# Kernel tuning notes

Measured on AMD Instinct MI355X. Metric: run time of the kernel, lower is better.

Reference implementation:

```python
import jax, jax.numpy as jnp
import numpy as np

N_BLOCK = 3; EMBED = 256; N_HEAD = 8; HEAD = EMBED // N_HEAD
N_AGENT = 8; SEQ = 256; BATCH = 64; ACT_DIM = 32
DECAY_SCALE = 1.0
EPS = 1e-6


def _decay_matrix():
    # Per-head decay kappas as in Mava Sable, decay over timesteps (pos // n_agent), causal mask.
    gammas = (1.0 - jnp.exp(jnp.linspace(jnp.log(1.0 / 32.0), jnp.log(1.0 / 512.0), N_HEAD))) * DECAY_SCALE
    t = (jnp.arange(SEQ) // N_AGENT).astype(jnp.float32)
    diff = t[:, None] - t[None, :]
    causal = jnp.arange(SEQ)[:, None] >= jnp.arange(SEQ)[None, :]
    return jnp.where(causal[None], gammas[:, None, None] ** diff[None], 0.0)  # [H,S,S]


def rmsnorm(x, scale):
    return x * jax.lax.rsqrt(jnp.mean(x * x, -1, keepdims=True) + EPS) * scale


def groupnorm(x, scale, bias):
    # GroupNorm with n_head groups over the feature dim, per position.
    B, S, E = x.shape
    xg = x.reshape(B, S, N_HEAD, HEAD)
    mu = xg.mean(-1, keepdims=True)
    var = ((xg - mu) ** 2).mean(-1, keepdims=True)
    xn = ((xg - mu) * jax.lax.rsqrt(var + 1e-5)).reshape(B, S, E)
    return xn * scale + bias


def retention(q_in, k_in, v_in, wq, wk, wv, wg, wo, gns, gnb, decay):
    # Parallel multi-scale retention: (Q K^T * D) V, groupnorm, swish gate from query input.
    B, S, E = q_in.shape
    q = (q_in @ wq).reshape(B, S, N_HEAD, HEAD).transpose(0, 2, 1, 3)
    k = (k_in @ wk).reshape(B, S, N_HEAD, HEAD).transpose(0, 2, 1, 3) / jnp.sqrt(jnp.float32(HEAD))
    v = (v_in @ wv).reshape(B, S, N_HEAD, HEAD).transpose(0, 2, 1, 3)
    scores = jnp.einsum('bhnd,bhmd->bhnm', q, k) * decay[None]
    ret = jnp.einsum('bhnm,bhmd->bhnd', scores, v)
    ret = groupnorm(ret.transpose(0, 2, 1, 3).reshape(B, S, E), gns, gnb)
    return (jax.nn.swish(q_in @ wg) * ret) @ wo


def swiglu(x, wg, w1, w2):
    return (jax.nn.swish(x @ wg) * (x @ w1)) @ w2


def forward(action, obs_rep, w_enc, ln0, wq1, wk1, wv1, wg1, wo1, gns1, gnb1, ln1,
            wq2, wk2, wv2, wg2, wo2, gns2, gnb2, ln2, swg, sw1, sw2, ln3,
            hw1, hb1, hln, hw2, hb2):
    decay = _decay_matrix()
    x = rmsnorm(jax.nn.gelu(action @ w_enc), ln0)
    for b in range(N_BLOCK):
        r1 = retention(x, x, x, wq1[b], wk1[b], wv1[b], wg1[b], wo1[b], gns1[b], gnb1[b], decay)
        x = rmsnorm(x + r1, ln1[b])
        r2 = retention(obs_rep, x, x, wq2[b], wk2[b], wv2[b], wg2[b], wo2[b], gns2[b], gnb2[b], decay)
        x = rmsnorm(obs_rep + r2, ln2[b])
        x = rmsnorm(x + swiglu(x, swg[b], sw1[b], sw2[b]), ln3[b])
    h = rmsnorm(jax.nn.gelu(x @ hw1 + hb1), hln)
    return h @ hw2 + hb2


def setup_inputs() -> dict:
    key = jax.random.key(0)
    ks = jax.random.split(key, 24)
    E, A, NB = EMBED, ACT_DIM, N_BLOCK
    s = 0.02
    return {
        'action': jax.random.uniform(ks[0], (BATCH, SEQ, A), jnp.float32),
        'obs_rep': jax.random.normal(ks[1], (BATCH, SEQ, E), jnp.float32),
        'w_enc': jax.random.normal(ks[2], (A, E), jnp.float32) * s,
        'ln0': jnp.ones((E,), jnp.float32),
        'wq1': jax.random.normal(ks[3], (NB, E, E), jnp.float32) * s,
        'wk1': jax.random.normal(ks[4], (NB, E, E), jnp.float32) * s,
        'wv1': jax.random.normal(ks[5], (NB, E, E), jnp.float32) * s,
        'wg1': jax.random.normal(ks[6], (NB, E, E), jnp.float32) * s,
        'wo1': jax.random.normal(ks[7], (NB, E, E), jnp.float32) * s,
        'gns1': jnp.ones((NB, E), jnp.float32),
        'gnb1': jnp.zeros((NB, E), jnp.float32),
        'ln1': jnp.ones((NB, E), jnp.float32),
        'wq2': jax.random.normal(ks[8], (NB, E, E), jnp.float32) * s,
        'wk2': jax.random.normal(ks[9], (NB, E, E), jnp.float32) * s,
        'wv2': jax.random.normal(ks[10], (NB, E, E), jnp.float32) * s,
        'wg2': jax.random.normal(ks[11], (NB, E, E), jnp.float32) * s,
        'wo2': jax.random.normal(ks[12], (NB, E, E), jnp.float32) * s,
        'gns2': jnp.ones((NB, E), jnp.float32),
        'gnb2': jnp.zeros((NB, E), jnp.float32),
        'ln2': jnp.ones((NB, E), jnp.float32),
        'swg': jax.random.normal(ks[13], (NB, E, E), jnp.float32) * s,
        'sw1': jax.random.normal(ks[14], (NB, E, E), jnp.float32) * s,
        'sw2': jax.random.normal(ks[15], (NB, E, E), jnp.float32) * s,
        'ln3': jnp.ones((NB, E), jnp.float32),
        'hw1': jax.random.normal(ks[16], (E, E), jnp.float32) * s,
        'hb1': jnp.zeros((E,), jnp.float32),
        'hln': jnp.ones((E,), jnp.float32),
        'hw2': jax.random.normal(ks[17], (E, A), jnp.float32) * s,
        'hb2': jnp.zeros((A,), jnp.float32),
    }


def reference(action, obs_rep, w_enc, ln0, wq1, wk1, wv1, wg1, wo1, gns1, gnb1, ln1,
              wq2, wk2, wv2, wg2, wo2, gns2, gnb2, ln2, swg, sw1, sw2, ln3,
              hw1, hb1, hln, hw2, hb2):
    return forward(action, obs_rep, w_enc, ln0, wq1, wk1, wv1, wg1, wo1, gns1, gnb1, ln1,
                   wq2, wk2, wv2, wg2, wo2, gns2, gnb2, ln2, swg, sw1, sw2, ln3,
                   hw1, hb1, hln, hw2, hb2)
```

## Files before the change

kernel.cpp:

```cpp
#include <hip/hip_runtime.h>
#include <cstdint>
#include <cmath>

typedef __attribute__((ext_vector_type(8))) short short8;
typedef __attribute__((ext_vector_type(4))) float floatx4;

#define DEV static __device__ __forceinline__

DEV float bf2f(uint16_t u) {
    union { uint32_t i; float f; } v; v.i = ((uint32_t)u) << 16; return v.f;
}
DEV uint16_t f2bf(float f) {
    union { float f; uint32_t i; } v; v.f = f;
    uint32_t r = (v.i + 0x7FFFu + ((v.i >> 16) & 1u)) >> 16;
    return (uint16_t)r;
}
DEV float swishf(float x) { return x / (1.f + __expf(-x)); }
DEV float geluf(float x) {
    const float c = 0.7978845608028654f;
    float t = tanhf(c * (x + 0.044715f * x * x * x));
    return 0.5f * x * (1.f + t);
}

#define CHUNK_E 8192
#define MAT_E   65536
#define APAD    264


struct TArg { const float* src[15]; };

__global__ __launch_bounds__(256) void tpose_k(TArg ta, uint16_t* __restrict__ arena) {
    int z = blockIdx.z;
    const float* src; uint16_t* dst;
    if (z == 0) {
        if (blockIdx.y) return;
        src = ta.src[0]; dst = arena;
    } else if (z <= 39) {
        int q = z - 1; int ti = q / 3, s = q % 3;
        src = ta.src[1 + ti] + (size_t)s * 65536;
        dst = arena + CHUNK_E + (size_t)(ti * 3 + s) * MAT_E;
    } else {
        src = ta.src[14]; dst = arena + CHUNK_E + (size_t)39 * MAT_E;
    }
    int k0 = blockIdx.y << 5;
    int n0 = blockIdx.x << 6;
    __shared__ __align__(16) uint16_t tile[32][72];
    int t = threadIdx.x;
    {
        int r = t >> 3, c = (t & 7) << 3;
        const float* s0 = src + (size_t)(k0 + r) * 256 + n0 + c;
        float4 f0 = *(const float4*)s0;
        float4 f1 = *(const float4*)(s0 + 4);
        tile[r][c + 0] = f2bf(f0.x); tile[r][c + 1] = f2bf(f0.y);
        tile[r][c + 2] = f2bf(f0.z); tile[r][c + 3] = f2bf(f0.w);
        tile[r][c + 4] = f2bf(f1.x); tile[r][c + 5] = f2bf(f1.y);
        tile[r][c + 6] = f2bf(f1.z); tile[r][c + 7] = f2bf(f1.w);
    }
    __syncthreads();
    {
        int n = t >> 2, c = (t & 3) << 3;
        uint16_t tmp[8];
#pragma unroll
        for (int j = 0; j < 8; ++j) tmp[j] = tile[c + j][n];
        *(uint4*)&dst[(size_t)(k0 >> 5) * CHUNK_E + (size_t)(n0 + n) * 32 + c] = *(uint4*)tmp;
    }
}

struct SegArgs {
    const float* action; const float* obs;
    uint16_t *actb, *obsb, *xb, *bq, *bk, *bv, *bg, *brg;
    const float *ln0, *hb1, *hln, *hw2, *hb2;
    float* outp;
    float l2g[8];
};

enum { EP_NONE = 0, EP_GELU_RMS = 1, EP_RESID_RMS = 2 };
enum { EP2_NONE = 0, EP2_SWIGLU = 1 };

template<int EPI, int K, int LDA, bool OG, int LDO, bool RL>
DEV void gemm_u(int m0,
                const uint16_t* __restrict__ A,
                const uint16_t* __restrict__ Wt,
                uint16_t* __restrict__ Og,
                uint16_t* __restrict__ Ol,
                const float* __restrict__ bias,
                const uint16_t* __restrict__ Rg,
                const uint16_t* __restrict__ Rl,
                const float* __restrict__ lnw,
                float (&rowsum)[8][32])
{
    const int t = threadIdx.x;
    const int w = t >> 6, lane = t & 63, l16 = lane & 15, lg = lane >> 4;
    constexpr int NC = K / 32;

    floatx4 acc[2][2];
#pragma unroll
    for (int i = 0; i < 2; ++i)
#pragma unroll
        for (int j = 0; j < 2; ++j) acc[i][j] = (floatx4){0.f, 0.f, 0.f, 0.f};

#pragma unroll
    for (int kc = 0; kc < NC; ++kc) {
        short8 aF[2], bF[2];
#pragma unroll
        for (int rt = 0; rt < 2; ++rt) {
            int row = (rt << 4) + l16;
            if constexpr (LDA != 0)
                aF[rt] = *(const short8*)(A + (size_t)row * LDA + (kc << 5) + (lg << 3));
            else
                aF[rt] = *(const short8*)(A + (size_t)(m0 + row) * K + (kc << 5) + (lg << 3));
        }
#pragma unroll
        for (int ct = 0; ct < 2; ++ct)
            bF[ct] = *(const short8*)(Wt + (size_t)kc * CHUNK_E +
                                      (size_t)((w << 5) + (ct << 4) + l16) * 32 + (lg << 3));
#pragma unroll
        for (int rt = 0; rt < 2; ++rt)
#pragma unroll
            for (int ct = 0; ct < 2; ++ct)
                acc[rt][ct] = __builtin_amdgcn_mfma_f32_16x16x32_bf16(
                    aF[rt], bF[ct], acc[rt][ct], 0, 0, 0);
    }

    float v[2][2][4];
#pragma unroll
    for (int rt = 0; rt < 2; ++rt)
#pragma unroll
        for (int ct = 0; ct < 2; ++ct)
#pragma unroll
            for (int r = 0; r < 4; ++r) {
                int row = (rt << 4) + (lg << 2) + r;
                int col = (w << 5) + (ct << 4) + l16;
                float x = acc[rt][ct][r];
                if constexpr (EPI == EP_GELU_RMS) {
                    if (bias) x += bias[col];
                    x = geluf(x);
                }
                if constexpr (EPI == EP_RESID_RMS) {
                    if constexpr (RL) x += bf2f(Rl[(size_t)row * APAD + col]);
                    else              x += bf2f(Rg[(size_t)(m0 + row) * 256 + col]);
                }
                v[rt][ct][r] = x;
            }

    if constexpr (EPI == EP_GELU_RMS || EPI == EP_RESID_RMS) {
#pragma unroll
        for (int rt = 0; rt < 2; ++rt)
#pragma unroll
            for (int r = 0; r < 4; ++r) {
                float p = v[rt][0][r] * v[rt][0][r] + v[rt][1][r] * v[rt][1][r];
                p += __shfl_xor(p, 1, 64); p += __shfl_xor(p, 2, 64);
                p += __shfl_xor(p, 4, 64); p += __shfl_xor(p, 8, 64);
                int row = (rt << 4) + (lg << 2) + r;
                if (l16 == 0) rowsum[w][row] = p;
            }
        __syncthreads();
#pragma unroll
        for (int rt = 0; rt < 2; ++rt)
#pragma unroll
            for (int r = 0; r < 4; ++r) {
                int row = (rt << 4) + (lg << 2) + r;
                float tot = rowsum[0][row] + rowsum[1][row] + rowsum[2][row] + rowsum[3][row]
                          + rowsum[4][row] + rowsum[5][row] + rowsum[6][row] + rowsum[7][row];
                float rn = rsqrtf(tot * (1.f / 256.f) + 1e-6f);
#pragma unroll
                for (int ct = 0; ct < 2; ++ct) {
                    int col = (w << 5) + (ct << 4) + l16;
                    uint16_t bb = f2bf(v[rt][ct][r] * rn * lnw[col]);
                    if constexpr (OG)
                        Og[(size_t)(m0 + row) * 256 + col] = bb;
                    if constexpr (LDO != 0)
                        Ol[(size_t)row * LDO + col] = bb;
                }
            }
        __syncthreads();
    } else {
#pragma unroll
        for (int rt = 0; rt < 2; ++rt)
#pragma unroll
            for (int ct = 0; ct < 2; ++ct)
#pragma unroll
                for (int r = 0; r < 4; ++r) {
                    int row = (rt << 4) + (lg << 2) + r;
                    int col = (w << 5) + (ct << 4) + l16;
                    uint16_t bb = f2bf(v[rt][ct][r]);
                    if constexpr (OG)
                        Og[(size_t)(m0 + row) * 256 + col] = bb;
                    if constexpr (LDO != 0)
                        Ol[(size_t)row * LDO + col] = bb;
                }
    }
}

template<int EPI, int LDA>
DEV void gemm2_u(int m0, const uint16_t* __restrict__ A,
                 const uint16_t* __restrict__ W1, const uint16_t* __restrict__ W2,
                 uint16_t* __restrict__ O1, uint16_t* __restrict__ O2,
                 uint16_t* __restrict__ Ol)
{
    const int t = threadIdx.x;
    const int w = t >> 6, lane = t & 63, l16 = lane & 15, lg = lane >> 4;

    floatx4 a1[2][2], a2[2][2];
#pragma unroll
    for (int i = 0; i < 2; ++i)
#pragma unroll
        for (int j = 0; j < 2; ++j) {
            a1[i][j] = (floatx4){0.f, 0.f, 0.f, 0.f};
            a2[i][j] = (floatx4){0.f, 0.f, 0.f, 0.f};
        }

#pragma unroll
    for (int kc = 0; kc < 8; ++kc) {
        short8 aF[2], b1[2], b2[2];
#pragma unroll
        for (int rt = 0; rt < 2; ++rt) {
            int row = (rt << 4) + l16;
            if constexpr (LDA != 0)
                aF[rt] = *(const short8*)(A + (size_t)row * LDA + (kc << 5) + (lg << 3));
            else
                aF[rt] = *(const short8*)(A + (size_t)(m0 + row) * 256 + (kc << 5) + (lg << 3));
        }
        size_t woff = (size_t)kc * CHUNK_E + (size_t)((w << 5) + l16) * 32 + (lg << 3);
#pragma unroll
        for (int ct = 0; ct < 2; ++ct) {
            b1[ct] = *(const short8*)(W1 + woff + (size_t)(ct << 4) * 32);
            b2[ct] = *(const short8*)(W2 + woff + (size_t)(ct << 4) * 32);
        }
#pragma unroll
        for (int rt = 0; rt < 2; ++rt)
#pragma unroll
            for (int ct = 0; ct < 2; ++ct) {
                a1[rt][ct] = __builtin_amdgcn_mfma_f32_16x16x32_bf16(aF[rt], b1[ct], a1[rt][ct], 0, 0, 0);
                a2[rt][ct] = __builtin_amdgcn_mfma_f32_16x16x32_bf16(aF[rt], b2[ct], a2[rt][ct], 0, 0, 0);
            }
    }

#pragma unroll
    for (int rt = 0; rt < 2; ++rt)
#pragma unroll
        for (int ct = 0; ct < 2; ++ct)
#pragma unroll
            for (int r = 0; r < 4; ++r) {
                int row = (rt << 4) + (lg << 2) + r;
                int col = (w << 5) + (ct << 4) + l16;
                if constexpr (EPI == EP2_NONE) {
                    size_t idx = (size_t)(m0 + row) * 256 + col;
                    O1[idx] = f2bf(a1[rt][ct][r]);
                    O2[idx] = f2bf(a2[rt][ct][r]);
                } else {
                    Ol[(size_t)row * APAD + col] = f2bf(swishf(a1[rt][ct][r]) * a2[rt][ct][r]);
                }
            }
}

DEV int rowbase(int blk) { return (blk & 63) * 256 + (blk >> 6) * 32; }


__global__ __launch_bounds__(512, 4) void seg0_k(SegArgs sa, const uint16_t* __restrict__ wenc,
                                                 const uint16_t* __restrict__ wq,
                                                 const uint16_t* __restrict__ wk,
                                                 const uint16_t* __restrict__ wv,
                                                 const uint16_t* __restrict__ wg)
{
    __shared__ float rowsum[8][32];
    __shared__ __align__(16) uint16_t actS[32][40];
    __shared__ __align__(16) uint16_t T0[32][APAD];
    const int t = threadIdx.x;
    const int m0 = rowbase(blockIdx.x);
    if (t < 256) {
        int r = t >> 3, c = (t & 7) << 2;
        float4 f = *(const float4*)(sa.action + (size_t)(m0 + r) * 32 + c);
        uint16_t tmp[4] = { f2bf(f.x), f2bf(f.y), f2bf(f.z), f2bf(f.w) };
        *(uint2*)&actS[r][c] = *(uint2*)tmp;
    }
    {
        const float4* ob = (const float4*)sa.obs + (size_t)m0 * 64;
        uint2* od = (uint2*)sa.obsb + (size_t)m0 * 64;
#pragma unroll
        for (int j = 0; j < 4; ++j) {
            float4 f = ob[(j << 9) + t];
            uint16_t tmp[4] = { f2bf(f.x), f2bf(f.y), f2bf(f.z), f2bf(f.w) };
            od[(j << 9) + t] = *(uint2*)tmp;
        }
    }
    __syncthreads();
    gemm_u<EP_GELU_RMS, 32, 40, true, APAD, false>(m0, &actS[0][0], wenc,
        sa.xb, &T0[0][0], nullptr, nullptr, nullptr, sa.ln0, rowsum);
    gemm2_u<EP2_NONE, APAD>(m0, &T0[0][0], wq, wk, sa.bq, sa.bk, nullptr);
    gemm2_u<EP2_NONE, APAD>(m0, &T0[0][0], wv, wg, sa.bv, sa.bg, nullptr);
}

__global__ __launch_bounds__(512, 4) void attn_k(SegArgs sa, const float* __restrict__ gns,
                                                 const float* __restrict__ gnb)
{
    __shared__ __align__(16) uint16_t QS[256][40];
    __shared__ __align__(16) uint16_t Ks[256][40];
    __shared__ __align__(16) uint16_t Vt[32][264];
    const int b = blockIdx.x & 63, h = blockIdx.x >> 6;
    const float l2g = sa.l2g[h];
    const int t = threadIdx.x, w = t >> 6, lane = t & 63, l16 = lane & 15, lg = lane >> 4;
    const size_t base = ((size_t)b * 256) * 256 + (size_t)h * 32;
    const uint16_t *q = sa.bq, *kbuf = sa.bk, *vbuf = sa.bv, *g = sa.bg;
    uint16_t* out = sa.brg;

    if (t < 256) {
        const uint4* qr = (const uint4*)(q + base + (size_t)t * 256);
        *(uint4*)&QS[t][0] = qr[0]; *(uint4*)&QS[t][8] = qr[1];
        *(uint4*)&QS[t][16] = qr[2]; *(uint4*)&QS[t][24] = qr[3];
        const uint4* kr = (const uint4*)(kbuf + base + (size_t)t * 256);
        *(uint4*)&Ks[t][0] = kr[0]; *(uint4*)&Ks[t][8] = kr[1];
        *(uint4*)&Ks[t][16] = kr[2]; *(uint4*)&Ks[t][24] = kr[3];
    } else {
        int c = t - 256;
        union { uint4 v4[4]; uint16_t u[32]; } vv;
        const uint4* vr = (const uint4*)(vbuf + base + (size_t)c * 256);
        vv.v4[0] = vr[0]; vv.v4[1] = vr[1]; vv.v4[2] = vr[2]; vv.v4[3] = vr[3];
#pragma unroll
        for (int d = 0; d < 32; ++d) Vt[d][c] = vv.u[d];
    }
    __syncthreads();

    short8 qF[2];
#pragma unroll
    for (int rt = 0; rt < 2; ++rt)
        qF[rt] = *(const short8*)&QS[(w << 5) + (rt << 4) + l16][lg << 3];

    floatx4 racc[2][2];
#pragma unroll
    for (int i = 0; i < 2; ++i) { racc[i][0] = (floatx4){0,0,0,0}; racc[i][1] = (floatx4){0,0,0,0}; }

    const float invsq = 0.17677669529663687f;
    const int jtmax = w;
    for (int jt = 0; jt <= jtmax; ++jt) {
        const int j0 = jt << 5;
        floatx4 sacc[2][2];
#pragma unroll
        for (int i = 0; i < 2; ++i) { sacc[i][0] = (floatx4){0,0,0,0}; sacc[i][1] = (floatx4){0,0,0,0}; }
        short8 kF[2];
#pragma unroll
        for (int ct = 0; ct < 2; ++ct)
            kF[ct] = *(const short8*)&Ks[j0 + (ct << 4) + l16][lg << 3];
#pragma unroll
        for (int rt = 0; rt < 2; ++rt)
#pragma unroll
            for (int ct = 0; ct < 2; ++ct)
                sacc[rt][ct] = __builtin_amdgcn_mfma_f32_16x16x32_bf16(
                    qF[rt], kF[ct], sacc[rt][ct], 0, 0, 0);
#pragma unroll
        for (int rt = 0; rt < 2; ++rt)
#pragma unroll
            for (int ct = 0; ct < 2; ++ct)
#pragma unroll
                for (int r = 0; r < 4; ++r) {
                    int row = (rt << 4) + (lg << 2) + r;
                    int i = (w << 5) + row;
                    int j = j0 + (ct << 4) + l16;
                    float svv = 0.f;
                    if (i >= j)
                        svv = sacc[rt][ct][r] * invsq *
                              exp2f((float)((i >> 3) - (j >> 3)) * l2g);
                    QS[(w << 5) + row][(ct << 4) + l16] = f2bf(svv);
                }
        short8 vF[2];
#pragma unroll
        for (int ct = 0; ct < 2; ++ct)
            vF[ct] = *(const short8*)&Vt[(ct << 4) + l16][j0 + (lg << 3)];
#pragma unroll
        for (int rt = 0; rt < 2; ++rt) {
            short8 sF = *(const short8*)&QS[(w << 5) + (rt << 4) + l16][lg << 3];
#pragma unroll
            for (int ct = 0; ct < 2; ++ct)
                racc[rt][ct] = __builtin_amdgcn_mfma_f32_16x16x32_bf16(
                    sF, vF[ct], racc[rt][ct], 0, 0, 0);
        }
    }

#pragma unroll
    for (int rt = 0; rt < 2; ++rt)
#pragma unroll
        for (int r = 0; r < 4; ++r) {
            float v0 = racc[rt][0][r], v1 = racc[rt][1][r];
            float s1 = v0 + v1, s2 = v0 * v0 + v1 * v1;
            s1 += __shfl_xor(s1, 1, 64); s2 += __shfl_xor(s2, 1, 64);
            s1 += __shfl_xor(s1, 2, 64); s2 += __shfl_xor(s2, 2, 64);
            s1 += __shfl_xor(s1, 4, 64); s2 += __shfl_xor(s2, 4, 64);
            s1 += __shfl_xor(s1, 8, 64); s2 += __shfl_xor(s2, 8, 64);
            float mu = s1 * (1.f / 32.f);
            float var = s2 * (1.f / 32.f) - mu * mu;
            float rstd = rsqrtf(var + 1e-5f);
            int srow = (w << 5) + (rt << 4) + (lg << 2) + r;
            size_t obase = ((size_t)b * 256 + srow) * 256 + (size_t)h * 32;
#pragma unroll
            for (int ct = 0; ct < 2; ++ct) {
                int d = (ct << 4) + l16;
                float x = ct ? v1 : v0;
                float y = (x - mu) * rstd * gns[h * 32 + d] + gnb[h * 32 + d];
                float gv = swishf(bf2f(g[obase + d]));
                out[obase + d] = f2bf(y * gv);
            }
        }
}

__global__ __launch_bounds__(512, 4) void g1_k(SegArgs sa,
    const uint16_t* __restrict__ wo, const float* __restrict__ ln1,
    const uint16_t* __restrict__ wq, const uint16_t* __restrict__ wk,
    const uint16_t* __restrict__ wv, const uint16_t* __restrict__ wg)
{
    __shared__ float rowsum[8][32];
    __shared__ __align__(16) uint16_t T0[32][APAD];
    const int m0 = rowbase(blockIdx.x);
    gemm_u<EP_RESID_RMS, 256, 0, false, APAD, false>(m0, sa.brg, wo,
        nullptr, &T0[0][0], nullptr, sa.xb, nullptr, ln1, rowsum);
    gemm2_u<EP2_NONE, APAD>(m0, &T0[0][0], wk, wv, sa.bk, sa.bv, nullptr);
    gemm2_u<EP2_NONE, 0>(m0, sa.obsb, wq, wg, sa.bq, sa.bg, nullptr);
}

__global__ __launch_bounds__(512, 4) void g2_k(SegArgs sa,
    const uint16_t* __restrict__ wo, const float* __restrict__ ln2,
    const uint16_t* __restrict__ wswg, const uint16_t* __restrict__ wsw1,
    const uint16_t* __restrict__ wsw2, const float* __restrict__ ln3,
    const uint16_t* __restrict__ nwq, const uint16_t* __restrict__ nwk,
    const uint16_t* __restrict__ nwv, const uint16_t* __restrict__ nwg)
{
    __shared__ float rowsum[8][32];
    __shared__ __align__(16) uint16_t T0[32][APAD];
    __shared__ __align__(16) uint16_t T1[32][APAD];
    const int m0 = rowbase(blockIdx.x);
    gemm_u<EP_RESID_RMS, 256, 0, false, APAD, false>(m0, sa.brg, wo,
        nullptr, &T0[0][0], nullptr, sa.obsb, nullptr, ln2, rowsum);
    gemm2_u<EP2_SWIGLU, APAD>(m0, &T0[0][0], wswg, wsw1, nullptr, nullptr, &T1[0][0]);
    __syncthreads();
    gemm_u<EP_RESID_RMS, 256, APAD, true, APAD, true>(m0, &T1[0][0], wsw2,
        sa.xb, &T0[0][0], nullptr, nullptr, &T0[0][0], ln3, rowsum);
    if (nwq) {
        gemm2_u<EP2_NONE, APAD>(m0, &T0[0][0], nwq, nwk, sa.bq, sa.bk, nullptr);
        gemm2_u<EP2_NONE, APAD>(m0, &T0[0][0], nwv, nwg, sa.bv, sa.bg, nullptr);
    }
}

__global__ __launch_bounds__(512, 4) void head_k(SegArgs sa, const uint16_t* __restrict__ hw1t)
{
    __shared__ float rowsum[8][32];
    __shared__ float w2s[8192];
    __shared__ __align__(16) uint16_t T0[32][APAD];
    const int t = threadIdx.x;
    const int m0 = rowbase(blockIdx.x);
#pragma unroll
    for (int j = 0; j < 16; ++j) w2s[(j << 9) + t] = sa.hw2[(j << 9) + t];
    gemm_u<EP_GELU_RMS, 256, 0, false, APAD, false>(m0, sa.xb, hw1t,
        nullptr, &T0[0][0], sa.hb1, nullptr, nullptr, sa.hln, rowsum);
    {
        int n = t & 31, rs = t >> 5;
#pragma unroll
        for (int rr = 0; rr < 2; ++rr) {
            int lrow = (rr << 4) + rs;
            float a0 = sa.hb2[n];
#pragma unroll 8
            for (int kk = 0; kk < 256; ++kk)
                a0 += bf2f(T0[lrow][kk]) * w2s[kk * 32 + n];
            sa.outp[(size_t)(m0 + lrow) * 32 + n] = a0;
        }
    }
}

extern "C" void kernel_launch(void* const* d_in, const int* in_sizes, int n_in,
                              void* d_out, int out_size, void* d_ws, size_t ws_size,
                              hipStream_t stream)
{
    const float* action = (const float*)d_in[0];
    const float* obs    = (const float*)d_in[1];
    const float* w_enc  = (const float*)d_in[2];
    const float* ln0    = (const float*)d_in[3];
    const float* wq1 = (const float*)d_in[4];
    const float* wk1 = (const float*)d_in[5];
    const float* wv1 = (const float*)d_in[6];
    const float* wg1 = (const float*)d_in[7];
    const float* wo1 = (const float*)d_in[8];
    const float* gns1 = (const float*)d_in[9];
    const float* gnb1 = (const float*)d_in[10];
    const float* ln1  = (const float*)d_in[11];
    const float* wq2 = (const float*)d_in[12];
    const float* wk2 = (const float*)d_in[13];
    const float* wv2 = (const float*)d_in[14];
    const float* wg2 = (const float*)d_in[15];
    const float* wo2 = (const float*)d_in[16];
    const float* gns2 = (const float*)d_in[17];
    const float* gnb2 = (const float*)d_in[18];
    const float* ln2  = (const float*)d_in[19];
    const float* swgp = (const float*)d_in[20];
    const float* sw1p = (const float*)d_in[21];
    const float* sw2p = (const float*)d_in[22];
    const float* ln3  = (const float*)d_in[23];
    const float* hw1  = (const float*)d_in[24];
    const float* hb1  = (const float*)d_in[25];
    const float* hln  = (const float*)d_in[26];
    const float* hw2  = (const float*)d_in[27];
    const float* hb2  = (const float*)d_in[28];

    char* ws = (char*)d_ws;
    uint16_t* wt   = (uint16_t*)(ws + 0);
    uint16_t* actb = (uint16_t*)(ws + 6291456);
    uint16_t* obsb = (uint16_t*)(ws + 7340032);
    uint16_t* xb   = (uint16_t*)(ws + 15728640);
    uint16_t* bq   = (uint16_t*)(ws + 24117248);
    uint16_t* bk   = (uint16_t*)(ws + 32505856);
    uint16_t* bv   = (uint16_t*)(ws + 40894464);
    uint16_t* bg   = (uint16_t*)(ws + 49283072);
    uint16_t* brg  = (uint16_t*)(ws + 57671680);

    uint16_t* wtenc = wt;
    uint16_t* hw1t  = wt + CHUNK_E + (size_t)39 * MAT_E;
    auto WTp = [&](int ti, int s) { return wt + CHUNK_E + (size_t)(ti * 3 + s) * MAT_E; };

    TArg ta;
    ta.src[0] = w_enc;
    ta.src[1] = wq1;  ta.src[2] = wk1;  ta.src[3] = wv1;  ta.src[4] = wg1;  ta.src[5] = wo1;
    ta.src[6] = wq2;  ta.src[7] = wk2;  ta.src[8] = wv2;  ta.src[9] = wg2;  ta.src[10] = wo2;
    ta.src[11] = swgp; ta.src[12] = sw1p; ta.src[13] = sw2p; ta.src[14] = hw1;
    tpose_k<<<dim3(4, 8, 41), 256, 0, stream>>>(ta, wt);

    SegArgs sa;
    sa.action = action; sa.obs = obs;
    sa.actb = actb; sa.obsb = obsb; sa.xb = xb;
    sa.bq = bq; sa.bk = bk; sa.bv = bv; sa.bg = bg; sa.brg = brg;
    sa.ln0 = ln0; sa.hb1 = hb1; sa.hln = hln; sa.hw2 = hw2; sa.hb2 = hb2;
    sa.outp = (float*)d_out;
    {
        const double a = log(1.0 / 32.0), bb = log(1.0 / 512.0);
        for (int hh = 0; hh < 8; ++hh) {
            double lg = a + (bb - a) * hh / 7.0;
            double gam = 1.0 - exp(lg);
            sa.l2g[hh] = (float)(log(gam) / log(2.0));
        }
    }

    dim3 GB(512), TB(512);
    seg0_k<<<GB, TB, 0, stream>>>(sa, wtenc, WTp(0, 0), WTp(1, 0), WTp(2, 0), WTp(3, 0));
    for (int b3 = 0; b3 < 3; ++b3) {
        attn_k<<<GB, TB, 0, stream>>>(sa, gns1 + b3 * 256, gnb1 + b3 * 256);
        g1_k<<<GB, TB, 0, stream>>>(sa, WTp(4, b3), ln1 + b3 * 256,
                                    WTp(5, b3), WTp(6, b3), WTp(7, b3), WTp(8, b3));
        attn_k<<<GB, TB, 0, stream>>>(sa, gns2 + b3 * 256, gnb2 + b3 * 256);
        g2_k<<<GB, TB, 0, stream>>>(sa, WTp(9, b3), ln2 + b3 * 256,
                                    WTp(10, b3), WTp(11, b3), WTp(12, b3), ln3 + b3 * 256,
                                    b3 < 2 ? WTp(0, b3 + 1) : nullptr,
                                    b3 < 2 ? WTp(1, b3 + 1) : nullptr,
                                    b3 < 2 ? WTp(2, b3 + 1) : nullptr,
                                    b3 < 2 ? WTp(3, b3 + 1) : nullptr);
    }
    head_k<<<GB, TB, 0, stream>>>(sa, hw1t);
}
```

Before: 555.1 us.

## Retile per-wave GEMM to 16x64 tiles and software-prefetch next K chunk

```diff
diff --git a/kernel.cpp b/kernel.cpp
--- a/kernel.cpp
+++ b/kernel.cpp
@@ -87,108 +87,111 @@
                 const uint16_t* __restrict__ Rg,
                 const uint16_t* __restrict__ Rl,
                 const float* __restrict__ lnw,
-                float (&rowsum)[8][32])
+                float (&rowsum)[4][32])
 {
     const int t = threadIdx.x;
     const int w = t >> 6, lane = t & 63, l16 = lane & 15, lg = lane >> 4;
+    const int rh = (w & 1) << 4;
+    const int cb = (w >> 1) << 6;
     constexpr int NC = K / 32;
 
-    floatx4 acc[2][2];
-#pragma unroll
-    for (int i = 0; i < 2; ++i)
-#pragma unroll
-        for (int j = 0; j < 2; ++j) acc[i][j] = (floatx4){0.f, 0.f, 0.f, 0.f};
+    floatx4 acc[4];
+#pragma unroll
+    for (int j = 0; j < 4; ++j) acc[j] = (floatx4){0.f, 0.f, 0.f, 0.f};
+
+    auto loadA = [&](int kc) -> short8 {
+        if constexpr (LDA != 0)
+            return *(const short8*)(A + (size_t)(rh + l16) * LDA + (kc << 5) + (lg << 3));
+        else
+            return *(const short8*)(A + (size_t)(m0 + rh + l16) * K + (kc << 5) + (lg << 3));
+    };
+    auto loadB = [&](int kc, int ct) -> short8 {
+        return *(const short8*)(Wt + (size_t)kc * CHUNK_E +
+                                (size_t)(cb + (ct << 4) + l16) * 32 + (lg << 3));
+    };
+
+    short8 aC, bC[4], aN, bN[4];
+    aC = loadA(0);
+#pragma unroll
+    for (int ct = 0; ct < 4; ++ct) bC[ct] = loadB(0, ct);
 
 #pragma unroll
     for (int kc = 0; kc < NC; ++kc) {
-        short8 aF[2], bF[2];
-#pragma unroll
-        for (int rt = 0; rt < 2; ++rt) {
-            int row = (rt << 4) + l16;
-            if constexpr (LDA != 0)
-                aF[rt] = *(const short8*)(A + (size_t)row * LDA + (kc << 5) + (lg << 3));
-            else
-                aF[rt] = *(const short8*)(A + (size_t)(m0 + row) * K + (kc << 5) + (lg << 3));
-        }
-#pragma unroll
-        for (int ct = 0; ct < 2; ++ct)
-            bF[ct] = *(const short8*)(Wt + (size_t)kc * CHUNK_E +
-                                      (size_t)((w << 5) + (ct << 4) + l16) * 32 + (lg << 3));
-#pragma unroll
-        for (int rt = 0; rt < 2; ++rt)
-#pragma unroll
-            for (int ct = 0; ct < 2; ++ct)
-                acc[rt][ct] = __builtin_amdgcn_mfma_f32_16x16x32_bf16(
-                    aF[rt], bF[ct], acc[rt][ct], 0, 0, 0);
-    }
-
-    float v[2][2][4];
-#pragma unroll
-    for (int rt = 0; rt < 2; ++rt)
-#pragma unroll
-        for (int ct = 0; ct < 2; ++ct)
-#pragma unroll
-            for (int r = 0; r < 4; ++r) {
-                int row = (rt << 4) + (lg << 2) + r;
-                int col = (w << 5) + (ct << 4) + l16;
-                float x = acc[rt][ct][r];
-                if constexpr (EPI == EP_GELU_RMS) {
-                    if (bias) x += bias[col];
-                    x = geluf(x);
-                }
-                if constexpr (EPI == EP_RESID_RMS) {
-                    if constexpr (RL) x += bf2f(Rl[(size_t)row * APAD + col]);
-                    else              x += bf2f(Rg[(size_t)(m0 + row) * 256 + col]);
-                }
-                v[rt][ct][r] = x;
+        if (kc + 1 < NC) {
+            aN = loadA(kc + 1);
+#pragma unroll
+            for (int ct = 0; ct < 4; ++ct) bN[ct] = loadB(kc + 1, ct);
+        }
+#pragma unroll
+        for (int ct = 0; ct < 4; ++ct)
+            acc[ct] = __builtin_amdgcn_mfma_f32_16x16x32_bf16(aC, bC[ct], acc[ct], 0, 0, 0);
+        if (kc + 1 < NC) {
+            aC = aN;
+#pragma unroll
+            for (int ct = 0; ct < 4; ++ct) bC[ct] = bN[ct];
+        }
+    }
+
+    float v[4][4];
+#pragma unroll
+    for (int ct = 0; ct < 4; ++ct)
+#pragma unroll
+        for (int r = 0; r < 4; ++r) {
+            int row = rh + (lg << 2) + r;
+            int col = cb + (ct << 4) + l16;
+            float x = acc[ct][r];
+            if constexpr (EPI == EP_GELU_RMS) {
+                if (bias) x += bias[col];
+                x = geluf(x);
             }
+            if constexpr (EPI == EP_RESID_RMS) {
+                if constexpr (RL) x += bf2f(Rl[(size_t)row * APAD + col]);
+                else              x += bf2f(Rg[(size_t)(m0 + row) * 256 + col]);
+            }
+            v[ct][r] = x;
+        }
 
     if constexpr (EPI == EP_GELU_RMS || EPI == EP_RESID_RMS) {
 #pragma unroll
-        for (int rt = 0; rt < 2; ++rt)
-#pragma unroll
-            for (int r = 0; r < 4; ++r) {
-                float p = v[rt][0][r] * v[rt][0][r] + v[rt][1][r] * v[rt][1][r];
-                p += __shfl_xor(p, 1, 64); p += __shfl_xor(p, 2, 64);
-                p += __shfl_xor(p, 4, 64); p += __shfl_xor(p, 8, 64);
-                int row = (rt << 4) + (lg << 2) + r;
-                if (l16 == 0) rowsum[w][row] = p;
+        for (int r = 0; r < 4; ++r) {
+            float p = 0.f;
+#pragma unroll
+            for (int ct = 0; ct < 4; ++ct) p += v[ct][r] * v[ct][r];
+            p += __shfl_xor(p, 1, 64); p += __shfl_xor(p, 2, 64);
+            p += __shfl_xor(p, 4, 64); p += __shfl_xor(p, 8, 64);
+            int row = rh + (lg << 2) + r;
+            if (l16 == 0) rowsum[w >> 1][row] = p;
+        }
+        __syncthreads();
+#pragma unroll
+        for (int r = 0; r < 4; ++r) {
+            int row = rh + (lg << 2) + r;
+            float tot = rowsum[0][row] + rowsum[1][row] + rowsum[2][row] + rowsum[3][row];
+            float rn = rsqrtf(tot * (1.f / 256.f) + 1e-6f);
+#pragma unroll
+            for (int ct = 0; ct < 4; ++ct) {
+                int col = cb + (ct << 4) + l16;
+                uint16_t bb = f2bf(v[ct][r] * rn * lnw[col]);
+                if constexpr (OG)
+                    Og[(size_t)(m0 + row) * 256 + col] = bb;
+                if constexpr (LDO != 0)
+                    Ol[(size_t)row * LDO + col] = bb;
             }
-        __syncthreads();
-#pragma unroll
-        for (int rt = 0; rt < 2; ++rt)
-#pragma unroll
-            for (int r = 0; r < 4; ++r) {
-                int row = (rt << 4) + (lg << 2) + r;
-                float tot = rowsum[0][row] + rowsum[1][row] + rowsum[2][row] + rowsum[3][row]
-                          + rowsum[4][row] + rowsum[5][row] + rowsum[6][row] + rowsum[7][row];
-                float rn = rsqrtf(tot * (1.f / 256.f) + 1e-6f);
-#pragma unroll
-                for (int ct = 0; ct < 2; ++ct) {
-                    int col = (w << 5) + (ct << 4) + l16;
-                    uint16_t bb = f2bf(v[rt][ct][r] * rn * lnw[col]);
-                    if constexpr (OG)
-                        Og[(size_t)(m0 + row) * 256 + col] = bb;
-                    if constexpr (LDO != 0)
-                        Ol[(size_t)row * LDO + col] = bb;
-                }
-            }
+        }
         __syncthreads();
     } else {
 #pragma unroll
-        for (int rt = 0; rt < 2; ++rt)
-#pragma unroll
-            for (int ct = 0; ct < 2; ++ct)
-#pragma unroll
-                for (int r = 0; r < 4; ++r) {
-                    int row = (rt << 4) + (lg << 2) + r;
-                    int col = (w << 5) + (ct << 4) + l16;
-                    uint16_t bb = f2bf(v[rt][ct][r]);
-                    if constexpr (OG)
-                        Og[(size_t)(m0 + row) * 256 + col] = bb;
-                    if constexpr (LDO != 0)
-                        Ol[(size_t)row * LDO + col] = bb;
-                }
+        for (int ct = 0; ct < 4; ++ct)
+#pragma unroll
+            for (int r = 0; r < 4; ++r) {
+                int row = rh + (lg << 2) + r;
+                int col = cb + (ct << 4) + l16;
+                uint16_t bb = f2bf(v[ct][r]);
+                if constexpr (OG)
+                    Og[(size_t)(m0 + row) * 256 + col] = bb;
+                if constexpr (LDO != 0)
+                    Ol[(size_t)row * LDO + col] = bb;
+            }
     }
 }
 
@@ -200,58 +203,50 @@
 {
     const int t = threadIdx.x;
     const int w = t >> 6, lane = t & 63, l16 = lane & 15, lg = lane >> 4;
-
-    floatx4 a1[2][2], a2[2][2];
-#pragma unroll
-    for (int i = 0; i < 2; ++i)
-#pragma unroll
-        for (int j = 0; j < 2; ++j) {
-            a1[i][j] = (floatx4){0.f, 0.f, 0.f, 0.f};
-            a2[i][j] = (floatx4){0.f, 0.f, 0.f, 0.f};
-        }
+    const int rh = (w & 1) << 4;
+    const int cb = (w >> 1) << 6;
+
+    floatx4 a1[4], a2[4];
+#pragma unroll
+    for (int j = 0; j < 4; ++j) {
+        a1[j] = (floatx4){0.f, 0.f, 0.f, 0.f};
+        a2[j] = (floatx4){0.f, 0.f, 0.f, 0.f};
+    }
 
 #pragma unroll
     for (int kc = 0; kc < 8; ++kc) {
-        short8 aF[2], b1[2], b2[2];
-#pragma unroll
-        for (int rt = 0; rt < 2; ++rt) {
-            int row = (rt << 4) + l16;
-            if constexpr (LDA != 0)
-                aF[rt] = *(const short8*)(A + (size_t)row * LDA + (kc << 5) + (lg << 3));
-            else
-                aF[rt] = *(const short8*)(A + (size_t)(m0 + row) * 256 + (kc << 5) + (lg << 3));
-        }
-        size_t woff = (size_t)kc * CHUNK_E + (size_t)((w << 5) + l16) * 32 + (lg << 3);
-#pragma unroll
-        for (int ct = 0; ct < 2; ++ct) {
+        short8 aF, b1[4], b2[4];
+        if constexpr (LDA != 0)
+            aF = *(const short8*)(A + (size_t)(rh + l16) * LDA + (kc << 5) + (lg << 3));
+        else
+            aF = *(const short8*)(A + (size_t)(m0 + rh + l16) * 256 + (kc << 5) + (lg << 3));
+        size_t woff = (size_t)kc * CHUNK_E + (size_t)(cb + l16) * 32 + (lg << 3);
+#pragma unroll
+        for (int ct = 0; ct < 4; ++ct) {
             b1[ct] = *(const short8*)(W1 + woff + (size_t)(ct << 4) * 32);
             b2[ct] = *(const short8*)(W2 + woff + (size_t)(ct << 4) * 32);
         }
 #pragma unroll
-        for (int rt = 0; rt < 2; ++rt)
-#pragma unroll
-            for (int ct = 0; ct < 2; ++ct) {
-                a1[rt][ct] = __builtin_amdgcn_mfma_f32_16x16x32_bf16(aF[rt], b1[ct], a1[rt][ct], 0, 0, 0);
-                a2[rt][ct] = __builtin_amdgcn_mfma_f32_16x16x32_bf16(aF[rt], b2[ct], a2[rt][ct], 0, 0, 0);
+        for (int ct = 0; ct < 4; ++ct) {
+            a1[ct] = __builtin_amdgcn_mfma_f32_16x16x32_bf16(aF, b1[ct], a1[ct], 0, 0, 0);
+            a2[ct] = __builtin_amdgcn_mfma_f32_16x16x32_bf16(aF, b2[ct], a2[ct], 0, 0, 0);
+        }
+    }
+
+#pragma unroll
+    for (int ct = 0; ct < 4; ++ct)
+#pragma unroll
+        for (int r = 0; r < 4; ++r) {
+            int row = rh + (lg << 2) + r;
+            int col = cb + (ct << 4) + l16;
+            if constexpr (EPI == EP2_NONE) {
+                size_t idx = (size_t)(m0 + row) * 256 + col;
+                O1[idx] = f2bf(a1[ct][r]);
+                O2[idx] = f2bf(a2[ct][r]);
+            } else {
+                Ol[(size_t)row * APAD + col] = f2bf(swishf(a1[ct][r]) * a2[ct][r]);
             }
-    }
-
-#pragma unroll
-    for (int rt = 0; rt < 2; ++rt)
-#pragma unroll
-        for (int ct = 0; ct < 2; ++ct)
-#pragma unroll
-            for (int r = 0; r < 4; ++r) {
-                int row = (rt << 4) + (lg << 2) + r;
-                int col = (w << 5) + (ct << 4) + l16;
-                if constexpr (EPI == EP2_NONE) {
-                    size_t idx = (size_t)(m0 + row) * 256 + col;
-                    O1[idx] = f2bf(a1[rt][ct][r]);
-                    O2[idx] = f2bf(a2[rt][ct][r]);
-                } else {
-                    Ol[(size_t)row * APAD + col] = f2bf(swishf(a1[rt][ct][r]) * a2[rt][ct][r]);
-                }
-            }
+        }
 }
 
 DEV int rowbase(int blk) { return (blk & 63) * 256 + (blk >> 6) * 32; }
@@ -263,7 +258,7 @@
                                                  const uint16_t* __restrict__ wv,
                                                  const uint16_t* __restrict__ wg)
 {
-    __shared__ float rowsum[8][32];
+    __shared__ float rowsum[4][32];
     __shared__ __align__(16) uint16_t actS[32][40];
     __shared__ __align__(16) uint16_t T0[32][APAD];
     const int t = threadIdx.x;
@@ -407,7 +402,7 @@
     const uint16_t* __restrict__ wq, const uint16_t* __restrict__ wk,
     const uint16_t* __restrict__ wv, const uint16_t* __restrict__ wg)
 {
-    __shared__ float rowsum[8][32];
+    __shared__ float rowsum[4][32];
     __shared__ __align__(16) uint16_t T0[32][APAD];
     const int m0 = rowbase(blockIdx.x);
     gemm_u<EP_RESID_RMS, 256, 0, false, APAD, false>(m0, sa.brg, wo,
@@ -423,7 +418,7 @@
     const uint16_t* __restrict__ nwq, const uint16_t* __restrict__ nwk,
     const uint16_t* __restrict__ nwv, const uint16_t* __restrict__ nwg)
 {
-    __shared__ float rowsum[8][32];
+    __shared__ float rowsum[4][32];
     __shared__ __align__(16) uint16_t T0[32][APAD];
     __shared__ __align__(16) uint16_t T1[32][APAD];
     const int m0 = rowbase(blockIdx.x);
@@ -441,7 +436,7 @@
 
 __global__ __launch_bounds__(512, 4) void head_k(SegArgs sa, const uint16_t* __restrict__ hw1t)
 {
-    __shared__ float rowsum[8][32];
+    __shared__ float rowsum[4][32];
     __shared__ float w2s[8192];
     __shared__ __align__(16) uint16_t T0[32][APAD];
     const int t = threadIdx.x;
```

Measured after the change: 624.5 us. 1.12x slower.

## Fuse QKVG projections into four-output GEMM and balance causal attention strips

Applied to the files above, without the earlier changes.

```diff
diff --git a/kernel.cpp b/kernel.cpp
--- a/kernel.cpp
+++ b/kernel.cpp
@@ -254,6 +254,128 @@
             }
 }
 
+template<int LDA>
+DEV void gemm4_u(int m0, const uint16_t* __restrict__ A,
+                 const uint16_t* __restrict__ W0, const uint16_t* __restrict__ W1,
+                 const uint16_t* __restrict__ W2, const uint16_t* __restrict__ W3,
+                 uint16_t* __restrict__ O0, uint16_t* __restrict__ O1,
+                 uint16_t* __restrict__ O2, uint16_t* __restrict__ O3)
+{
+    const int t = threadIdx.x;
+    const int w = t >> 6, lane = t & 63, l16 = lane & 15, lg = lane >> 4;
+    const uint16_t* Wm[4] = {W0, W1, W2, W3};
+    uint16_t* Om[4] = {O0, O1, O2, O3};
+
+    floatx4 acc[4][2][2];
+#pragma unroll
+    for (int m = 0; m < 4; ++m)
+#pragma unroll
+        for (int i = 0; i < 2; ++i)
+#pragma unroll
+            for (int j = 0; j < 2; ++j) acc[m][i][j] = (floatx4){0.f, 0.f, 0.f, 0.f};
+
+#pragma unroll
+    for (int kc = 0; kc < 8; ++kc) {
+        short8 aF[2];
+#pragma unroll
+        for (int rt = 0; rt < 2; ++rt) {
+            int row = (rt << 4) + l16;
+            if constexpr (LDA != 0)
+                aF[rt] = *(const short8*)(A + (size_t)row * LDA + (kc << 5) + (lg << 3));
+            else
+                aF[rt] = *(const short8*)(A + (size_t)(m0 + row) * 256 + (kc << 5) + (lg << 3));
+        }
+        size_t woff = (size_t)kc * CHUNK_E + (size_t)((w << 5) + l16) * 32 + (lg << 3);
+        short8 bF[4][2];
+#pragma unroll
+        for (int m = 0; m < 4; ++m)
+#pragma unroll
+            for (int ct = 0; ct < 2; ++ct)
+                bF[m][ct] = *(const short8*)(Wm[m] + woff + (size_t)(ct << 4) * 32);
+#pragma unroll
+        for (int m = 0; m < 4; ++m)
+#pragma unroll
+            for (int rt = 0; rt < 2; ++rt)
+#pragma unroll
+                for (int ct = 0; ct < 2; ++ct)
+                    acc[m][rt][ct] = __builtin_amdgcn_mfma_f32_16x16x32_bf16(
+                        aF[rt], bF[m][ct], acc[m][rt][ct], 0, 0, 0);
+    }
+
+#pragma unroll
+    for (int m = 0; m < 4; ++m)
+#pragma unroll
+        for (int rt = 0; rt < 2; ++rt)
+#pragma unroll
+            for (int ct = 0; ct < 2; ++ct)
+#pragma unroll
+                for (int r = 0; r < 4; ++r) {
+                    int row = (rt << 4) + (lg << 2) + r;
+                    int col = (w << 5) + (ct << 4) + l16;
+                    Om[m][(size_t)(m0 + row) * 256 + col] = f2bf(acc[m][rt][ct][r]);
+                }
+}
+
+template<int LDA1>
+DEV void gemm22_u(int m0, const uint16_t* __restrict__ A1, const uint16_t* __restrict__ A2,
+                  const uint16_t* __restrict__ W0, const uint16_t* __restrict__ W1,
+                  const uint16_t* __restrict__ W2, const uint16_t* __restrict__ W3,
+                  uint16_t* __restrict__ O0, uint16_t* __restrict__ O1,
+                  uint16_t* __restrict__ O2, uint16_t* __restrict__ O3)
+{
+    const int t = threadIdx.x;
+    const int w = t >> 6, lane = t & 63, l16 = lane & 15, lg = lane >> 4;
+    const uint16_t* Wm[4] = {W0, W1, W2, W3};
+    uint16_t* Om[4] = {O0, O1, O2, O3};
+
+    floatx4 acc[4][2][2];
+#pragma unroll
+    for (int m = 0; m < 4; ++m)
+#pragma unroll
+        for (int i = 0; i < 2; ++i)
+#pragma unroll
+            for (int j = 0; j < 2; ++j) acc[m][i][j] = (floatx4){0.f, 0.f, 0.f, 0.f};
+
+#pragma unroll
+    for (int kc = 0; kc < 8; ++kc) {
+        short8 a1F[2], a2F[2];
+#pragma unroll
+        for (int rt = 0; rt < 2; ++rt) {
+            int row = (rt << 4) + l16;
+            a1F[rt] = *(const short8*)(A1 + (size_t)row * LDA1 + (kc << 5) + (lg << 3));
+            a2F[rt] = *(const short8*)(A2 + (size_t)(m0 + row) * 256 + (kc << 5) + (lg << 3));
+        }
+        size_t woff = (size_t)kc * CHUNK_E + (size_t)((w << 5) + l16) * 32 + (lg << 3);
+        short8 bF[4][2];
+#pragma unroll
+        for (int m = 0; m < 4; ++m)
+#pragma unroll
+            for (int ct = 0; ct < 2; ++ct)
+                bF[m][ct] = *(const short8*)(Wm[m] + woff + (size_t)(ct << 4) * 32);
+#pragma unroll
+        for (int m = 0; m < 4; ++m)
+#pragma unroll
+            for (int rt = 0; rt < 2; ++rt)
+#pragma unroll
+                for (int ct = 0; ct < 2; ++ct)
+                    acc[m][rt][ct] = __builtin_amdgcn_mfma_f32_16x16x32_bf16(
+                        (m < 2) ? a1F[rt] : a2F[rt], bF[m][ct], acc[m][rt][ct], 0, 0, 0);
+    }
+
+#pragma unroll
+    for (int m = 0; m < 4; ++m)
+#pragma unroll
+        for (int rt = 0; rt < 2; ++rt)
+#pragma unroll
+            for (int ct = 0; ct < 2; ++ct)
+#pragma unroll
+                for (int r = 0; r < 4; ++r) {
+                    int row = (rt << 4) + (lg << 2) + r;
+                    int col = (w << 5) + (ct << 4) + l16;
+                    Om[m][(size_t)(m0 + row) * 256 + col] = f2bf(acc[m][rt][ct][r]);
+                }
+}
+
 DEV int rowbase(int blk) { return (blk & 63) * 256 + (blk >> 6) * 32; }
 
 
@@ -287,8 +409,7 @@
     __syncthreads();
     gemm_u<EP_GELU_RMS, 32, 40, true, APAD, false>(m0, &actS[0][0], wenc,
         sa.xb, &T0[0][0], nullptr, nullptr, nullptr, sa.ln0, rowsum);
-    gemm2_u<EP2_NONE, APAD>(m0, &T0[0][0], wq, wk, sa.bq, sa.bk, nullptr);
-    gemm2_u<EP2_NONE, APAD>(m0, &T0[0][0], wv, wg, sa.bv, sa.bg, nullptr);
+    gemm4_u<APAD>(m0, &T0[0][0], wq, wk, wv, wg, sa.bq, sa.bk, sa.bv, sa.bg);
 }
 
 __global__ __launch_bounds__(512, 4) void attn_k(SegArgs sa, const float* __restrict__ gns,
@@ -321,66 +442,61 @@
     }
     __syncthreads();
 
-    short8 qF[2];
-#pragma unroll
-    for (int rt = 0; rt < 2; ++rt)
-        qF[rt] = *(const short8*)&QS[(w << 5) + (rt << 4) + l16][lg << 3];
-
-    floatx4 racc[2][2];
-#pragma unroll
-    for (int i = 0; i < 2; ++i) { racc[i][0] = (floatx4){0,0,0,0}; racc[i][1] = (floatx4){0,0,0,0}; }
+    const int iA = w, iB = 15 - w;
+    short8 qFA = *(const short8*)&QS[(iA << 4) + l16][lg << 3];
+    short8 qFB = *(const short8*)&QS[(iB << 4) + l16][lg << 3];
 
     const float invsq = 0.17677669529663687f;
-    const int jtmax = w;
-    for (int jt = 0; jt <= jtmax; ++jt) {
-        const int j0 = jt << 5;
-        floatx4 sacc[2][2];
-#pragma unroll
-        for (int i = 0; i < 2; ++i) { sacc[i][0] = (floatx4){0,0,0,0}; sacc[i][1] = (floatx4){0,0,0,0}; }
-        short8 kF[2];
-#pragma unroll
-        for (int ct = 0; ct < 2; ++ct)
-            kF[ct] = *(const short8*)&Ks[j0 + (ct << 4) + l16][lg << 3];
-#pragma unroll
-        for (int rt = 0; rt < 2; ++rt)
-#pragma unroll
-            for (int ct = 0; ct < 2; ++ct)
-                sacc[rt][ct] = __builtin_amdgcn_mfma_f32_16x16x32_bf16(
-                    qF[rt], kF[ct], sacc[rt][ct], 0, 0, 0);
-#pragma unroll
-        for (int rt = 0; rt < 2; ++rt)
+
+    floatx4 raccA[2], raccB[2];
+    raccA[0] = (floatx4){0,0,0,0}; raccA[1] = (floatx4){0,0,0,0};
+    raccB[0] = (floatx4){0,0,0,0}; raccB[1] = (floatx4){0,0,0,0};
+
+    auto do_strip = [&](int si, short8 qF, floatx4 (&racc)[2]) {
+        const int jtmax = ((si << 4) + 15) >> 5;
+        for (int jt = 0; jt <= jtmax; ++jt) {
+            const int j0 = jt << 5;
+            floatx4 sacc[2];
+            sacc[0] = (floatx4){0,0,0,0}; sacc[1] = (floatx4){0,0,0,0};
+            short8 kF[2];
+#pragma unroll
+            for (int ct = 0; ct < 2; ++ct)
+                kF[ct] = *(const short8*)&Ks[j0 + (ct << 4) + l16][lg << 3];
+#pragma unroll
+            for (int ct = 0; ct < 2; ++ct)
+                sacc[ct] = __builtin_amdgcn_mfma_f32_16x16x32_bf16(
+                    qF, kF[ct], sacc[ct], 0, 0, 0);
 #pragma unroll
             for (int ct = 0; ct < 2; ++ct)
 #pragma unroll
                 for (int r = 0; r < 4; ++r) {
-                    int row = (rt << 4) + (lg << 2) + r;
-                    int i = (w << 5) + row;
+                    int row16 = (lg << 2) + r;
+                    int i = (si << 4) + row16;
                     int j = j0 + (ct << 4) + l16;
                     float svv = 0.f;
                     if (i >= j)
-                        svv = sacc[rt][ct][r] * invsq *
+                        svv = sacc[ct][r] * invsq *
                               exp2f((float)((i >> 3) - (j >> 3)) * l2g);
-                    QS[(w << 5) + row][(ct << 4) + l16] = f2bf(svv);
-                }
-        short8 vF[2];
-#pragma unroll
-        for (int ct = 0; ct < 2; ++ct)
-            vF[ct] = *(const short8*)&Vt[(ct << 4) + l16][j0 + (lg << 3)];
-#pragma unroll
-        for (int rt = 0; rt < 2; ++rt) {
-            short8 sF = *(const short8*)&QS[(w << 5) + (rt << 4) + l16][lg << 3];
-#pragma unroll
-            for (int ct = 0; ct < 2; ++ct)
-                racc[rt][ct] = __builtin_amdgcn_mfma_f32_16x16x32_bf16(
-                    sF, vF[ct], racc[rt][ct], 0, 0, 0);
-        }
-    }
-
-#pragma unroll
-    for (int rt = 0; rt < 2; ++rt)
+                    QS[(si << 4) + row16][(ct << 4) + l16] = f2bf(svv);
+                }
+            short8 vF[2];
+#pragma unroll
+            for (int ct = 0; ct < 2; ++ct)
+                vF[ct] = *(const short8*)&Vt[(ct << 4) + l16][j0 + (lg << 3)];
+            short8 sF = *(const short8*)&QS[(si << 4) + l16][lg << 3];
+#pragma unroll
+            for (int ct = 0; ct < 2; ++ct)
+                racc[ct] = __builtin_amdgcn_mfma_f32_16x16x32_bf16(
+                    sF, vF[ct], racc[ct], 0, 0, 0);
+        }
+    };
+    do_strip(iA, qFA, raccA);
+    do_strip(iB, qFB, raccB);
+
+    auto epi = [&](int si, floatx4 (&racc)[2]) {
 #pragma unroll
         for (int r = 0; r < 4; ++r) {
-            float v0 = racc[rt][0][r], v1 = racc[rt][1][r];
+            float v0 = racc[0][r], v1 = racc[1][r];
             float s1 = v0 + v1, s2 = v0 * v0 + v1 * v1;
             s1 += __shfl_xor(s1, 1, 64); s2 += __shfl_xor(s2, 1, 64);
             s1 += __shfl_xor(s1, 2, 64); s2 += __shfl_xor(s2, 2, 64);
@@ -389,7 +505,7 @@
             float mu = s1 * (1.f / 32.f);
             float var = s2 * (1.f / 32.f) - mu * mu;
             float rstd = rsqrtf(var + 1e-5f);
-            int srow = (w << 5) + (rt << 4) + (lg << 2) + r;
+            int srow = (si << 4) + (lg << 2) + r;
             size_t obase = ((size_t)b * 256 + srow) * 256 + (size_t)h * 32;
 #pragma unroll
             for (int ct = 0; ct < 2; ++ct) {
@@ -400,6 +516,9 @@
                 out[obase + d] = f2bf(y * gv);
             }
         }
+    };
+    epi(iA, raccA);
+    epi(iB, raccB);
 }
 
 __global__ __launch_bounds__(512, 4) void g1_k(SegArgs sa,
@@ -412,8 +531,8 @@
     const int m0 = rowbase(blockIdx.x);
     gemm_u<EP_RESID_RMS, 256, 0, false, APAD, false>(m0, sa.brg, wo,
         nullptr, &T0[0][0], nullptr, sa.xb, nullptr, ln1, rowsum);
-    gemm2_u<EP2_NONE, APAD>(m0, &T0[0][0], wk, wv, sa.bk, sa.bv, nullptr);
-    gemm2_u<EP2_NONE, 0>(m0, sa.obsb, wq, wg, sa.bq, sa.bg, nullptr);
+    gemm22_u<APAD>(m0, &T0[0][0], sa.obsb, wk, wv, wq, wg,
+                   sa.bk, sa.bv, sa.bq, sa.bg);
 }
 
 __global__ __launch_bounds__(512, 4) void g2_k(SegArgs sa,
@@ -434,8 +553,7 @@
     gemm_u<EP_RESID_RMS, 256, APAD, true, APAD, true>(m0, &T1[0][0], wsw2,
         sa.xb, &T0[0][0], nullptr, nullptr, &T0[0][0], ln3, rowsum);
     if (nwq) {
-        gemm2_u<EP2_NONE, APAD>(m0, &T0[0][0], nwq, nwk, sa.bq, sa.bk, nullptr);
-        gemm2_u<EP2_NONE, APAD>(m0, &T0[0][0], nwv, nwg, sa.bv, sa.bg, nullptr);
+        gemm4_u<APAD>(m0, &T0[0][0], nwq, nwk, nwv, nwg, sa.bq, sa.bk, sa.bv, sa.bg);
     }
 }
 
```

New measurement: 566.3 us. 1.02x slower.
